# Optimization experiments

Measured on AMD Instinct MI355X. Metric: run time of the kernel, lower is better.

## Reference

```python
import jax, jax.numpy as jnp
import numpy as np

N_NODES = 50000
N_EDGES = 800000
IN_FEATS = 128
OUT_FEATS = 128


def setup_inputs() -> dict:
    key = jax.random.key(0)
    k1, k2, k3, k4, k5 = jax.random.split(key, 5)
    # xavier_uniform for W
    limit = float(np.sqrt(6.0 / (IN_FEATS + OUT_FEATS)))
    W = jax.random.uniform(k2, (IN_FEATS, OUT_FEATS), jnp.float32, -limit, limit)
    return {
        "feat": jax.random.normal(k1, (N_NODES, IN_FEATS), jnp.float32),
        "W": W,
        "b": jnp.zeros((OUT_FEATS,), jnp.float32),
        "edge_w": jax.random.uniform(k3, (N_EDGES,), jnp.float32),
        "edge_src": jax.random.randint(k4, (N_EDGES,), 0, N_NODES),
        "edge_dst": jax.random.randint(k5, (N_EDGES,), 0, N_NODES),
    }


def reference(feat, W, b, edge_w, edge_src, edge_dst):
    N = feat.shape[0]
    ones = jnp.ones(edge_src.shape[0], feat.dtype)
    # norm == 'both': scale src features by out_degree^{-1/2}
    out_deg = jnp.clip(jax.ops.segment_sum(ones, edge_src, num_segments=N), 1.0)
    feat = feat * (out_deg ** -0.5)[:, None]  # [N, in]
    # in_feats (128) is NOT > out_feats (128): aggregate first, then matmul
    msgs = feat[edge_src] * edge_w[:, None]  # [E, in] (u_mul_e)
    agg = jax.ops.segment_sum(msgs, edge_dst, num_segments=N)  # [N, in] (sum)
    rst = agg @ W  # [N, out]
    # dst-side normalization: in_degree^{-1/2}
    in_deg = jnp.clip(jax.ops.segment_sum(ones, edge_dst, num_segments=N), 1.0)
    rst = rst * (in_deg ** -0.5)[:, None] + b
    return rst
```

## Files before the change

kernel.cpp:

```cpp
#include <hip/hip_runtime.h>
#include <math.h>

#define N_NODES 50000
#define N_EDGES 800000
#define F 128
#define CAP 64
#define NB 64
#define EPB 12500
#define HALF 25000
#define SLOTS 12500


__global__ __launch_bounds__(256) void hist_kernel(
    const int* __restrict__ src, unsigned* __restrict__ partial) {
    __shared__ unsigned h[SLOTS];
    int b = blockIdx.x, tid = threadIdx.x;
    int e0 = b * EPB;
    int e1 = e0 + EPB;
    if (e1 > N_EDGES) e1 = N_EDGES;
    for (int h2 = 0; h2 < 2; ++h2) {
        for (int j = tid; j < SLOTS; j += 256) h[j] = 0;
        __syncthreads();
        int base = h2 * HALF;
        for (int e = e0 + tid; e < e1; e += 256) {
            int s = src[e];
            unsigned us = (unsigned)(s - base);
            if (us < HALF)
                atomicAdd(&h[us >> 1], 1u << ((s & 1) * 16));
        }
        __syncthreads();
        unsigned* po = partial + ((size_t)h2 * NB + b) * SLOTS;
        for (int j = tid; j < SLOTS; j += 256) po[j] = h[j];
        __syncthreads();
    }
}

__global__ __launch_bounds__(256) void reduce_kernel(
    const unsigned* __restrict__ partial, float* __restrict__ inv_od) {
    int t = blockIdx.x * blockDim.x + threadIdx.x;
    if (t >= 2 * SLOTS) return;
    int h2 = t / SLOTS, j = t - h2 * SLOTS;
    const unsigned* p = partial + (size_t)h2 * NB * SLOTS + j;
    unsigned lo = 0, hi = 0;
    for (int b = 0; b < NB; ++b) {
        unsigned v = p[(size_t)b * SLOTS];
        lo += v & 0xFFFFu;
        hi += v >> 16;
    }
    int n0 = h2 * HALF + 2 * j;
    inv_od[n0] = rsqrtf(fmaxf((float)lo, 1.0f));
    inv_od[n0 + 1] = rsqrtf(fmaxf((float)hi, 1.0f));
}

__global__ __launch_bounds__(256) void place_kernel(
    const int* __restrict__ src, const int* __restrict__ dst,
    const float* __restrict__ edge_w,
    int* __restrict__ cnt, int2* __restrict__ meta) {
    int e = blockIdx.x * blockDim.x + threadIdx.x;
    if (e >= N_EDGES) return;
    int s = src[e];
    int d = dst[e];
    int pos = atomicAdd(&cnt[d], 1);
    if (pos < CAP)
        meta[(size_t)d * CAP + pos] = make_int2(s, __float_as_int(edge_w[e]));
}

__global__ __launch_bounds__(256) void gather_kernel(
    const float* __restrict__ feat, const int* __restrict__ cnt,
    const float* __restrict__ inv_od, const int2* __restrict__ meta,
    float* __restrict__ agg) {
    int wid = (blockIdx.x * blockDim.x + threadIdx.x) >> 6;
    if (wid >= N_NODES) return;
    int lane = threadIdx.x & 63;
    int half = lane >> 5, l = lane & 31;
    int c = cnt[wid];
    if (c > CAP) c = CAP;
    const int2* m = meta + (size_t)wid * CAP;
    float4 acc = make_float4(0.f, 0.f, 0.f, 0.f);
    int j = half;
    for (; j + 2 < c; j += 4) {
        int2 m0 = m[j];
        int2 m1 = m[j + 2];
        float w0 = __int_as_float(m0.y) * inv_od[m0.x];
        float w1 = __int_as_float(m1.y) * inv_od[m1.x];
        float4 v0 = ((const float4*)(feat + (size_t)m0.x * F))[l];
        float4 v1 = ((const float4*)(feat + (size_t)m1.x * F))[l];
        acc.x += w0 * v0.x; acc.y += w0 * v0.y;
        acc.z += w0 * v0.z; acc.w += w0 * v0.w;
        acc.x += w1 * v1.x; acc.y += w1 * v1.y;
        acc.z += w1 * v1.z; acc.w += w1 * v1.w;
    }
    for (; j < c; j += 2) {
        int2 m0 = m[j];
        float w0 = __int_as_float(m0.y) * inv_od[m0.x];
        float4 v0 = ((const float4*)(feat + (size_t)m0.x * F))[l];
        acc.x += w0 * v0.x; acc.y += w0 * v0.y;
        acc.z += w0 * v0.z; acc.w += w0 * v0.w;
    }
    acc.x += __shfl_xor(acc.x, 32, 64);
    acc.y += __shfl_xor(acc.y, 32, 64);
    acc.z += __shfl_xor(acc.z, 32, 64);
    acc.w += __shfl_xor(acc.w, 32, 64);
    if (half == 0)
        ((float4*)(agg + (size_t)wid * F))[l] = acc;
}

__global__ __launch_bounds__(256) void gemm_inplace(
    const float* __restrict__ W, const float* __restrict__ bias,
    const int* __restrict__ cnt, float* __restrict__ io) {
    __shared__ float As[64][36];
    __shared__ float Ws[32][128];

    int tid = threadIdx.x;
    int row0 = blockIdx.x * 64;
    int tx = tid & 15, ty = tid >> 4;

    float acc[4][8] = {{0.f}};
    for (int kt = 0; kt < 4; ++kt) {
        __syncthreads();
#pragma unroll
        for (int p = 0; p < 2; ++p) {
            int q = tid + p * 256;
            int r = q >> 3, c4 = q & 7;
            int gr = row0 + r;
            float4 v = make_float4(0.f, 0.f, 0.f, 0.f);
            if (gr < N_NODES)
                v = ((const float4*)(io + (size_t)gr * F + kt * 32))[c4];
            *(float4*)&As[r][c4 * 4] = v;
        }
#pragma unroll
        for (int p = 0; p < 4; ++p) {
            int q = tid + p * 256;
            int r = q >> 5, c4 = q & 31;
            *(float4*)&Ws[r][c4 * 4] = ((const float4*)(W + (size_t)(kt * 32 + r) * F))[c4];
        }
        __syncthreads();
#pragma unroll
        for (int k = 0; k < 32; ++k) {
            float a[4];
#pragma unroll
            for (int i = 0; i < 4; ++i) a[i] = As[ty * 4 + i][k];
            float4 b0 = *(float4*)&Ws[k][tx * 4];
            float4 b1 = *(float4*)&Ws[k][64 + tx * 4];
#pragma unroll
            for (int i = 0; i < 4; ++i) {
                acc[i][0] += a[i] * b0.x;
                acc[i][1] += a[i] * b0.y;
                acc[i][2] += a[i] * b0.z;
                acc[i][3] += a[i] * b0.w;
                acc[i][4] += a[i] * b1.x;
                acc[i][5] += a[i] * b1.y;
                acc[i][6] += a[i] * b1.z;
                acc[i][7] += a[i] * b1.w;
            }
        }
    }

#pragma unroll
    for (int i = 0; i < 4; ++i) {
        int gr = row0 + ty * 4 + i;
        if (gr >= N_NODES) continue;
        float sc = rsqrtf(fmaxf((float)cnt[gr], 1.0f));
        float4 o0, o1;
        o0.x = acc[i][0] * sc + bias[tx * 4 + 0];
        o0.y = acc[i][1] * sc + bias[tx * 4 + 1];
        o0.z = acc[i][2] * sc + bias[tx * 4 + 2];
        o0.w = acc[i][3] * sc + bias[tx * 4 + 3];
        o1.x = acc[i][4] * sc + bias[64 + tx * 4 + 0];
        o1.y = acc[i][5] * sc + bias[64 + tx * 4 + 1];
        o1.z = acc[i][6] * sc + bias[64 + tx * 4 + 2];
        o1.w = acc[i][7] * sc + bias[64 + tx * 4 + 3];
        ((float4*)(io + (size_t)gr * F))[tx] = o0;
        ((float4*)(io + (size_t)gr * F))[16 + tx] = o1;
    }
}

extern "C" void kernel_launch(void* const* d_in, const int* in_sizes, int n_in,
                              void* d_out, int out_size, void* d_ws, size_t ws_size,
                              hipStream_t stream) {
    const float* feat   = (const float*)d_in[0];
    const float* W      = (const float*)d_in[1];
    const float* bias   = (const float*)d_in[2];
    const float* edge_w = (const float*)d_in[3];
    const int* edge_src = (const int*)d_in[4];
    const int* edge_dst = (const int*)d_in[5];
    float* out = (float*)d_out;

    int2* meta     = (int2*)d_ws;
    int* cnt       = (int*)((char*)d_ws + (size_t)N_NODES * CAP * sizeof(int2));
    float* inv_od  = (float*)(cnt + N_NODES);
    unsigned* part = (unsigned*)d_ws;

    hipMemsetAsync(cnt, 0, (size_t)N_NODES * sizeof(int), stream);

    hist_kernel<<<NB, 256, 0, stream>>>(edge_src, part);
    reduce_kernel<<<(2 * SLOTS + 255) / 256, 256, 0, stream>>>(part, inv_od);

    place_kernel<<<(N_EDGES + 255) / 256, 256, 0, stream>>>(
        edge_src, edge_dst, edge_w, cnt, meta);

    gather_kernel<<<(N_NODES * 64 + 255) / 256, 256, 0, stream>>>(
        feat, cnt, inv_od, meta, out);

    gemm_inplace<<<(N_NODES + 63) / 64, 256, 0, stream>>>(
        W, bias, cnt, out);
}
```

Before: 249.0 us.

## Tune histogram grid, fold cnt zeroing, unroll gather, prefetch GEMM tiles

The histogram now runs over more blocks with fewer edges each. The separate memset of the in-degree counters is removed, and reduce_kernel zeroes them instead. The gather loop is unrolled to four edges per half-wave so more feature loads are in flight. The GEMM moves to 32-row tiles with register prefetch of the next K-slice, overlapping global loads with compute and doubling the block count for occupancy. The risks are a larger partial-histogram buffer and more gemm blocks that each reload all of W.

```diff
diff --git a/kernel.cpp b/kernel.cpp
--- a/kernel.cpp
+++ b/kernel.cpp
@@ -5,8 +5,8 @@
 #define N_EDGES 800000
 #define F 128
 #define CAP 64
-#define NB 64
-#define EPB 12500
+#define NB 256
+#define EPB 3125
 #define HALF 25000
 #define SLOTS 12500
 
@@ -36,7 +36,8 @@
 }
 
 __global__ __launch_bounds__(256) void reduce_kernel(
-    const unsigned* __restrict__ partial, float* __restrict__ inv_od) {
+    const unsigned* __restrict__ partial, float* __restrict__ inv_od,
+    int* __restrict__ cnt) {
     int t = blockIdx.x * blockDim.x + threadIdx.x;
     if (t >= 2 * SLOTS) return;
     int h2 = t / SLOTS, j = t - h2 * SLOTS;
@@ -50,6 +51,8 @@
     int n0 = h2 * HALF + 2 * j;
     inv_od[n0] = rsqrtf(fmaxf((float)lo, 1.0f));
     inv_od[n0 + 1] = rsqrtf(fmaxf((float)hi, 1.0f));
+    cnt[n0] = 0;
+    cnt[n0 + 1] = 0;
 }
 
 __global__ __launch_bounds__(256) void place_kernel(
@@ -78,17 +81,27 @@
     const int2* m = meta + (size_t)wid * CAP;
     float4 acc = make_float4(0.f, 0.f, 0.f, 0.f);
     int j = half;
-    for (; j + 2 < c; j += 4) {
+    for (; j + 6 < c; j += 8) {
         int2 m0 = m[j];
         int2 m1 = m[j + 2];
+        int2 m2 = m[j + 4];
+        int2 m3 = m[j + 6];
         float w0 = __int_as_float(m0.y) * inv_od[m0.x];
         float w1 = __int_as_float(m1.y) * inv_od[m1.x];
+        float w2 = __int_as_float(m2.y) * inv_od[m2.x];
+        float w3 = __int_as_float(m3.y) * inv_od[m3.x];
         float4 v0 = ((const float4*)(feat + (size_t)m0.x * F))[l];
         float4 v1 = ((const float4*)(feat + (size_t)m1.x * F))[l];
+        float4 v2 = ((const float4*)(feat + (size_t)m2.x * F))[l];
+        float4 v3 = ((const float4*)(feat + (size_t)m3.x * F))[l];
         acc.x += w0 * v0.x; acc.y += w0 * v0.y;
         acc.z += w0 * v0.z; acc.w += w0 * v0.w;
         acc.x += w1 * v1.x; acc.y += w1 * v1.y;
         acc.z += w1 * v1.z; acc.w += w1 * v1.w;
+        acc.x += w2 * v2.x; acc.y += w2 * v2.y;
+        acc.z += w2 * v2.z; acc.w += w2 * v2.w;
+        acc.x += w3 * v3.x; acc.y += w3 * v3.y;
+        acc.z += w3 * v3.z; acc.w += w3 * v3.w;
     }
     for (; j < c; j += 2) {
         int2 m0 = m[j];
@@ -108,57 +121,62 @@
 __global__ __launch_bounds__(256) void gemm_inplace(
     const float* __restrict__ W, const float* __restrict__ bias,
     const int* __restrict__ cnt, float* __restrict__ io) {
-    __shared__ float As[64][36];
+    __shared__ float As[32][36];
     __shared__ float Ws[32][128];
 
     int tid = threadIdx.x;
-    int row0 = blockIdx.x * 64;
+    int row0 = blockIdx.x * 32;
     int tx = tid & 15, ty = tid >> 4;
 
-    float acc[4][8] = {{0.f}};
+    int ar = tid >> 3, ac4 = tid & 7;
+    int wr = tid >> 5, wc4 = tid & 31;
+    int garow = row0 + ar;
+
+    float4 pa;
+    float4 pw[4];
+    pa = make_float4(0.f, 0.f, 0.f, 0.f);
+    if (garow < N_NODES)
+        pa = ((const float4*)(io + (size_t)garow * F))[ac4];
+#pragma unroll
+    for (int p = 0; p < 4; ++p)
+        pw[p] = ((const float4*)(W + (size_t)(wr + p * 8) * F))[wc4];
+
+    float acc[2][8] = {{0.f}};
     for (int kt = 0; kt < 4; ++kt) {
-        __syncthreads();
-#pragma unroll
-        for (int p = 0; p < 2; ++p) {
-            int q = tid + p * 256;
-            int r = q >> 3, c4 = q & 7;
-            int gr = row0 + r;
-            float4 v = make_float4(0.f, 0.f, 0.f, 0.f);
-            if (gr < N_NODES)
-                v = ((const float4*)(io + (size_t)gr * F + kt * 32))[c4];
-            *(float4*)&As[r][c4 * 4] = v;
+        *(float4*)&As[ar][ac4 * 4] = pa;
+#pragma unroll
+        for (int p = 0; p < 4; ++p)
+            *(float4*)&Ws[wr + p * 8][wc4 * 4] = pw[p];
+        __syncthreads();
+        if (kt < 3) {
+            pa = make_float4(0.f, 0.f, 0.f, 0.f);
+            if (garow < N_NODES)
+                pa = ((const float4*)(io + (size_t)garow * F + (kt + 1) * 32))[ac4];
+#pragma unroll
+            for (int p = 0; p < 4; ++p)
+                pw[p] = ((const float4*)(W + (size_t)((kt + 1) * 32 + wr + p * 8) * F))[wc4];
         }
 #pragma unroll
-        for (int p = 0; p < 4; ++p) {
-            int q = tid + p * 256;
-            int r = q >> 5, c4 = q & 31;
-            *(float4*)&Ws[r][c4 * 4] = ((const float4*)(W + (size_t)(kt * 32 + r) * F))[c4];
-        }
-        __syncthreads();
-#pragma unroll
         for (int k = 0; k < 32; ++k) {
-            float a[4];
-#pragma unroll
-            for (int i = 0; i < 4; ++i) a[i] = As[ty * 4 + i][k];
+            float a0 = As[ty * 2 + 0][k];
+            float a1 = As[ty * 2 + 1][k];
             float4 b0 = *(float4*)&Ws[k][tx * 4];
             float4 b1 = *(float4*)&Ws[k][64 + tx * 4];
-#pragma unroll
-            for (int i = 0; i < 4; ++i) {
-                acc[i][0] += a[i] * b0.x;
-                acc[i][1] += a[i] * b0.y;
-                acc[i][2] += a[i] * b0.z;
-                acc[i][3] += a[i] * b0.w;
-                acc[i][4] += a[i] * b1.x;
-                acc[i][5] += a[i] * b1.y;
-                acc[i][6] += a[i] * b1.z;
-                acc[i][7] += a[i] * b1.w;
-            }
+            acc[0][0] += a0 * b0.x; acc[0][1] += a0 * b0.y;
+            acc[0][2] += a0 * b0.z; acc[0][3] += a0 * b0.w;
+            acc[0][4] += a0 * b1.x; acc[0][5] += a0 * b1.y;
+            acc[0][6] += a0 * b1.z; acc[0][7] += a0 * b1.w;
+            acc[1][0] += a1 * b0.x; acc[1][1] += a1 * b0.y;
+            acc[1][2] += a1 * b0.z; acc[1][3] += a1 * b0.w;
+            acc[1][4] += a1 * b1.x; acc[1][5] += a1 * b1.y;
+            acc[1][6] += a1 * b1.z; acc[1][7] += a1 * b1.w;
         }
-    }
-
-#pragma unroll
-    for (int i = 0; i < 4; ++i) {
-        int gr = row0 + ty * 4 + i;
+        __syncthreads();
+    }
+
+#pragma unroll
+    for (int i = 0; i < 2; ++i) {
+        int gr = row0 + ty * 2 + i;
         if (gr >= N_NODES) continue;
         float sc = rsqrtf(fmaxf((float)cnt[gr], 1.0f));
         float4 o0, o1;
@@ -191,10 +209,8 @@
     float* inv_od  = (float*)(cnt + N_NODES);
     unsigned* part = (unsigned*)d_ws;
 
-    hipMemsetAsync(cnt, 0, (size_t)N_NODES * sizeof(int), stream);
-
     hist_kernel<<<NB, 256, 0, stream>>>(edge_src, part);
-    reduce_kernel<<<(2 * SLOTS + 255) / 256, 256, 0, stream>>>(part, inv_od);
+    reduce_kernel<<<(2 * SLOTS + 255) / 256, 256, 0, stream>>>(part, inv_od, cnt);
 
     place_kernel<<<(N_EDGES + 255) / 256, 256, 0, stream>>>(
         edge_src, edge_dst, edge_w, cnt, meta);
@@ -202,6 +218,6 @@
     gather_kernel<<<(N_NODES * 64 + 255) / 256, 256, 0, stream>>>(
         feat, cnt, inv_od, meta, out);
 
-    gemm_inplace<<<(N_NODES + 63) / 64, 256, 0, stream>>>(
+    gemm_inplace<<<(N_NODES + 31) / 32, 256, 0, stream>>>(
         W, bias, cnt, out);
 }
```

Measured after the change: 254.7 us. 2.3% more time.

## Widen histogram grid, fold count reset into reduce, split gather, prefetch GEMM tiles

Applied to the files above, without the earlier changes.

The histogram kernel now uses 256 blocks instead of 64, which gives more parallelism but makes the reduce pass read four times as many partials. The memset of the counts is removed and the counts are zeroed inside reduce_kernel instead, saving one launch. The gather is split into two launches over the two halves of the nodes. The GEMM now prefetches the next K-tile into registers while computing the current one, to hide global-load latency.

```diff
diff --git a/kernel.cpp b/kernel.cpp
--- a/kernel.cpp
+++ b/kernel.cpp
@@ -5,8 +5,8 @@
 #define N_EDGES 800000
 #define F 128
 #define CAP 64
-#define NB 64
-#define EPB 12500
+#define NB 256
+#define EPB 3125
 #define HALF 25000
 #define SLOTS 12500
 
@@ -36,7 +36,8 @@
 }
 
 __global__ __launch_bounds__(256) void reduce_kernel(
-    const unsigned* __restrict__ partial, float* __restrict__ inv_od) {
+    const unsigned* __restrict__ partial, float* __restrict__ inv_od,
+    int* __restrict__ cnt) {
     int t = blockIdx.x * blockDim.x + threadIdx.x;
     if (t >= 2 * SLOTS) return;
     int h2 = t / SLOTS, j = t - h2 * SLOTS;
@@ -50,6 +51,8 @@
     int n0 = h2 * HALF + 2 * j;
     inv_od[n0] = rsqrtf(fmaxf((float)lo, 1.0f));
     inv_od[n0 + 1] = rsqrtf(fmaxf((float)hi, 1.0f));
+    cnt[n0] = 0;
+    cnt[n0 + 1] = 0;
 }
 
 __global__ __launch_bounds__(256) void place_kernel(
@@ -68,9 +71,9 @@
 __global__ __launch_bounds__(256) void gather_kernel(
     const float* __restrict__ feat, const int* __restrict__ cnt,
     const float* __restrict__ inv_od, const int2* __restrict__ meta,
-    float* __restrict__ agg) {
-    int wid = (blockIdx.x * blockDim.x + threadIdx.x) >> 6;
-    if (wid >= N_NODES) return;
+    float* __restrict__ agg, int node_base, int node_end) {
+    int wid = node_base + ((blockIdx.x * blockDim.x + threadIdx.x) >> 6);
+    if (wid >= node_end) return;
     int lane = threadIdx.x & 63;
     int half = lane >> 5, l = lane & 31;
     int c = cnt[wid];
@@ -115,26 +118,37 @@
     int row0 = blockIdx.x * 64;
     int tx = tid & 15, ty = tid >> 4;
 
+    int ar = tid >> 3, ac = tid & 7;
+    int g0 = row0 + ar, g1 = row0 + 32 + ar;
+    int wr = tid >> 5, wc = tid & 31;
+
+    float4 pa0, pa1, pw[4];
+    pa0 = make_float4(0.f, 0.f, 0.f, 0.f);
+    pa1 = make_float4(0.f, 0.f, 0.f, 0.f);
+    if (g0 < N_NODES) pa0 = ((const float4*)(io + (size_t)g0 * F))[ac];
+    if (g1 < N_NODES) pa1 = ((const float4*)(io + (size_t)g1 * F))[ac];
+#pragma unroll
+    for (int p = 0; p < 4; ++p)
+        pw[p] = ((const float4*)(W + (size_t)(wr + p * 8) * F))[wc];
+
     float acc[4][8] = {{0.f}};
     for (int kt = 0; kt < 4; ++kt) {
-        __syncthreads();
-#pragma unroll
-        for (int p = 0; p < 2; ++p) {
-            int q = tid + p * 256;
-            int r = q >> 3, c4 = q & 7;
-            int gr = row0 + r;
-            float4 v = make_float4(0.f, 0.f, 0.f, 0.f);
-            if (gr < N_NODES)
-                v = ((const float4*)(io + (size_t)gr * F + kt * 32))[c4];
-            *(float4*)&As[r][c4 * 4] = v;
+        *(float4*)&As[ar][ac * 4] = pa0;
+        *(float4*)&As[32 + ar][ac * 4] = pa1;
+#pragma unroll
+        for (int p = 0; p < 4; ++p)
+            *(float4*)&Ws[wr + p * 8][wc * 4] = pw[p];
+        __syncthreads();
+        if (kt < 3) {
+            int ko = (kt + 1) * 32;
+            pa0 = make_float4(0.f, 0.f, 0.f, 0.f);
+            pa1 = make_float4(0.f, 0.f, 0.f, 0.f);
+            if (g0 < N_NODES) pa0 = ((const float4*)(io + (size_t)g0 * F + ko))[ac];
+            if (g1 < N_NODES) pa1 = ((const float4*)(io + (size_t)g1 * F + ko))[ac];
+#pragma unroll
+            for (int p = 0; p < 4; ++p)
+                pw[p] = ((const float4*)(W + (size_t)(ko + wr + p * 8) * F))[wc];
         }
-#pragma unroll
-        for (int p = 0; p < 4; ++p) {
-            int q = tid + p * 256;
-            int r = q >> 5, c4 = q & 31;
-            *(float4*)&Ws[r][c4 * 4] = ((const float4*)(W + (size_t)(kt * 32 + r) * F))[c4];
-        }
-        __syncthreads();
 #pragma unroll
         for (int k = 0; k < 32; ++k) {
             float a[4];
@@ -144,16 +158,13 @@
             float4 b1 = *(float4*)&Ws[k][64 + tx * 4];
 #pragma unroll
             for (int i = 0; i < 4; ++i) {
-                acc[i][0] += a[i] * b0.x;
-                acc[i][1] += a[i] * b0.y;
-                acc[i][2] += a[i] * b0.z;
-                acc[i][3] += a[i] * b0.w;
-                acc[i][4] += a[i] * b1.x;
-                acc[i][5] += a[i] * b1.y;
-                acc[i][6] += a[i] * b1.z;
-                acc[i][7] += a[i] * b1.w;
+                acc[i][0] += a[i] * b0.x; acc[i][1] += a[i] * b0.y;
+                acc[i][2] += a[i] * b0.z; acc[i][3] += a[i] * b0.w;
+                acc[i][4] += a[i] * b1.x; acc[i][5] += a[i] * b1.y;
+                acc[i][6] += a[i] * b1.z; acc[i][7] += a[i] * b1.w;
             }
         }
+        __syncthreads();
     }
 
 #pragma unroll
@@ -191,16 +202,16 @@
     float* inv_od  = (float*)(cnt + N_NODES);
     unsigned* part = (unsigned*)d_ws;
 
-    hipMemsetAsync(cnt, 0, (size_t)N_NODES * sizeof(int), stream);
-
     hist_kernel<<<NB, 256, 0, stream>>>(edge_src, part);
-    reduce_kernel<<<(2 * SLOTS + 255) / 256, 256, 0, stream>>>(part, inv_od);
+    reduce_kernel<<<(2 * SLOTS + 255) / 256, 256, 0, stream>>>(part, inv_od, cnt);
 
     place_kernel<<<(N_EDGES + 255) / 256, 256, 0, stream>>>(
         edge_src, edge_dst, edge_w, cnt, meta);
 
-    gather_kernel<<<(N_NODES * 64 + 255) / 256, 256, 0, stream>>>(
-        feat, cnt, inv_od, meta, out);
+    gather_kernel<<<(HALF * 64) / 256, 256, 0, stream>>>(
+        feat, cnt, inv_od, meta, out, 0, HALF);
+    gather_kernel<<<(HALF * 64) / 256, 256, 0, stream>>>(
+        feat, cnt, inv_od, meta, out, HALF, N_NODES);
 
     gemm_inplace<<<(N_NODES + 63) / 64, 256, 0, stream>>>(
         W, bias, cnt, out);
```

New measurement: 254.5 us. +2.2%, slower.
